# Optimization experiments

Measured on AMD Instinct MI355X. Metric: run time of the kernel, lower is better.

## Reference

```python
import jax, jax.numpy as jnp
import numpy as np

GRAPH_DIM = 512
LLM_DIM = 4096
N_HEADS = 8
D_KEYS = 128
DK_H = N_HEADS * D_KEYS  # 1024


def setup_inputs() -> dict:
    key = jax.random.key(0)
    ks = jax.random.split(key, 12)
    B, L, S = 8, 1024, 1000
    sc = 0.02
    return {
        "target_embedding": jax.random.normal(ks[0], (B, L, GRAPH_DIM), jnp.float32),
        "source_embedding": jax.random.normal(ks[1], (S, LLM_DIM), jnp.float32),
        "value_embedding": jax.random.normal(ks[2], (S, LLM_DIM), jnp.float32),
        # weights stored as [in, out] (pre-transposed vs torch Linear)
        "Wq": jax.random.normal(ks[3], (GRAPH_DIM, DK_H), jnp.float32) * sc,
        "bq": jnp.zeros((DK_H,), jnp.float32),
        "Wk": jax.random.normal(ks[4], (LLM_DIM, DK_H), jnp.float32) * sc,
        "bk": jnp.zeros((DK_H,), jnp.float32),
        "Wv": jax.random.normal(ks[5], (LLM_DIM, DK_H), jnp.float32) * sc,
        "bv": jnp.zeros((DK_H,), jnp.float32),
        "Wo": jax.random.normal(ks[6], (DK_H, LLM_DIM), jnp.float32) * sc,
        "bo": jnp.zeros((LLM_DIM,), jnp.float32),
    }


def reference(target_embedding, source_embedding, value_embedding,
              Wq, bq, Wk, bk, Wv, bv, Wo, bo):
    B, L, _ = target_embedding.shape
    S, _ = source_embedding.shape
    H, E = N_HEADS, D_KEYS
    q = (target_embedding @ Wq + bq).reshape(B, L, H, E)   # blhe
    k = (source_embedding @ Wk + bk).reshape(S, H, E)      # she (batch-shared)
    v = (value_embedding @ Wv + bv).reshape(S, H, E)       # she (batch-shared)
    scale = 1.0 / jnp.sqrt(jnp.asarray(E, q.dtype))
    scores = jnp.einsum('blhe,she->bhls', q, k)            # [B,H,L,S]
    A = jax.nn.softmax(scale * scores, axis=-1)            # dropout = identity (eval)
    out = jnp.einsum('bhls,she->blhe', A, v).reshape(B, L, H * E)
    return out @ Wo + bo                                   # [B,L,llm_dim]
```

## Files before the change

kernel.cpp:

```cpp
#include <hip/hip_runtime.h>
#include <cstdint>
#include <cstddef>

typedef __bf16 bf16;
typedef __bf16 bf16x4 __attribute__((ext_vector_type(4)));
typedef __bf16 bf16x8 __attribute__((ext_vector_type(8)));
typedef float f32x4 __attribute__((ext_vector_type(4)));


__device__ __forceinline__ void gload_lds16(const void* g, void* l) {
    typedef __attribute__((address_space(1))) void gv;
    typedef __attribute__((address_space(3))) void lv;
    __builtin_amdgcn_global_load_lds((gv*)g, (lv*)l, 16, 0, 0);
}

__global__ __launch_bounds__(256) void cast3_f32_bf16(
    const float* __restrict__ in0, bf16* __restrict__ out0,
    const float* __restrict__ in1, bf16* __restrict__ out1,
    const float* __restrict__ in2, bf16* __restrict__ out2)
{
    const int which = blockIdx.y;
    const float* in = which == 0 ? in0 : which == 1 ? in1 : in2;
    bf16* out       = which == 0 ? out0 : which == 1 ? out1 : out2;
    const size_t n_in = which == 0 ? (size_t)8192 * 512 : (size_t)1000 * 4096;

    const size_t i = ((size_t)blockIdx.x * 256 + threadIdx.x) * 8;
    f32x4 a = (f32x4){0.f, 0.f, 0.f, 0.f};
    f32x4 b = (f32x4){0.f, 0.f, 0.f, 0.f};
    if (i < n_in) {
        a = *(const f32x4*)(in + i);
        b = *(const f32x4*)(in + i + 4);
    }
    bf16x8 o;
    o[0] = (bf16)a[0]; o[1] = (bf16)a[1]; o[2] = (bf16)a[2]; o[3] = (bf16)a[3];
    o[4] = (bf16)b[0]; o[5] = (bf16)b[1]; o[6] = (bf16)b[2]; o[7] = (bf16)b[3];
    *(bf16x8*)(out + i) = o;
}

__global__ __launch_bounds__(256) void transpose_cast(
    const float* __restrict__ in, bf16* __restrict__ out, int R, int C)
{
    __shared__ bf16 tile[32][33];
    const int tx = threadIdx.x & 31, ty = threadIdx.x >> 5;
    const int c0 = blockIdx.x * 32, r0 = blockIdx.y * 32;
    #pragma unroll
    for (int i = ty; i < 32; i += 8)
        tile[i][tx] = (bf16)in[(size_t)(r0 + i) * C + (c0 + tx)];
    __syncthreads();
    #pragma unroll
    for (int i = ty; i < 32; i += 8)
        out[(size_t)(c0 + i) * R + (r0 + tx)] = tile[tx][i];
}

__global__ __launch_bounds__(256) void gemm_bt(
    const bf16* __restrict__ A, const bf16* __restrict__ Bt,
    const float* __restrict__ bias, void* __restrict__ Cv,
    int M, int N, int K, int lda, int ldb, int ldc, int outF32)
{
    __shared__ __align__(16) bf16 As[128 * 32];
    __shared__ __align__(16) bf16 Bs[128 * 32];

    const int tid = threadIdx.x;
    const int w = tid >> 6, ln = tid & 63;
    const int bm = blockIdx.y, bn = blockIdx.x;
    const int wm = (w >> 1) * 64, wn = (w & 1) * 64;
    const int rgrp = ln >> 4, cl = ln & 15;

    f32x4 acc[4][4];
    #pragma unroll
    for (int mt = 0; mt < 4; ++mt)
        #pragma unroll
        for (int nt = 0; nt < 4; ++nt)
            acc[mt][nt] = (f32x4){0.f, 0.f, 0.f, 0.f};

    for (int k0 = 0; k0 < K; k0 += 32) {
        #pragma unroll
        for (int j = 0; j < 2; ++j) {
            const int t2 = tid + 256 * j;
            int arow = bm * 128 + (t2 >> 2);
            if (arow > M - 1) arow = M - 1;
            const bf16* ag = A + (size_t)arow * lda + k0 + (t2 & 3) * 8;
            gload_lds16(ag, (char*)As + j * 4096 + w * 1024);
            const int brow = bn * 128 + (t2 >> 2);
            const bf16* bg = Bt + (size_t)brow * ldb + k0 + (t2 & 3) * 8;
            gload_lds16(bg, (char*)Bs + j * 4096 + w * 1024);
        }
        __syncthreads();

        bf16x8 af[4], bfr[4];
        #pragma unroll
        for (int mt = 0; mt < 4; ++mt)
            af[mt] = *(const bf16x8*)(As + (wm + mt * 16 + cl) * 32 + rgrp * 8);
        #pragma unroll
        for (int nt = 0; nt < 4; ++nt)
            bfr[nt] = *(const bf16x8*)(Bs + (wn + nt * 16 + cl) * 32 + rgrp * 8);
        #pragma unroll
        for (int mt = 0; mt < 4; ++mt)
            #pragma unroll
            for (int nt = 0; nt < 4; ++nt)
                acc[mt][nt] = __builtin_amdgcn_mfma_f32_16x16x32_bf16(
                    bfr[nt], af[mt], acc[mt][nt], 0, 0, 0);
        __syncthreads();
    }

    #pragma unroll
    for (int nt = 0; nt < 4; ++nt) {
        const int col0 = bn * 128 + wn + nt * 16 + rgrp * 4;
        const f32x4 bv4 = bias ? *(const f32x4*)(bias + col0)
                               : (f32x4){0.f, 0.f, 0.f, 0.f};
        #pragma unroll
        for (int mt = 0; mt < 4; ++mt) {
            const int row = bm * 128 + wm + mt * 16 + cl;
            if (row < M) {
                const f32x4 v = acc[mt][nt] + bv4;
                if (outF32) {
                    __builtin_nontemporal_store(
                        v, (f32x4*)((float*)Cv + (size_t)row * ldc + col0));
                } else {
                    bf16x4 h;
                    h[0] = (bf16)v[0]; h[1] = (bf16)v[1];
                    h[2] = (bf16)v[2]; h[3] = (bf16)v[3];
                    *(bf16x4*)((bf16*)Cv + (size_t)row * ldc + col0) = h;
                }
            }
        }
    }
}

__global__ __launch_bounds__(256) void gemm_kv(
    const bf16* __restrict__ A0, const bf16* __restrict__ Bt0,
    const float* __restrict__ b0, bf16* __restrict__ C0,
    const bf16* __restrict__ A1, const bf16* __restrict__ Bt1,
    const float* __restrict__ b1, bf16* __restrict__ C1)
{
    const int sel = blockIdx.z;
    const bf16* A  = sel ? A1 : A0;
    const bf16* Bt = sel ? Bt1 : Bt0;
    const float* bias = sel ? b1 : b0;
    bf16* Cv = sel ? C1 : C0;
    const int transC = sel;
    const int M = 1024, K = 4096, lda = 4096, ldb = 4096, ldc = 1024;

    __shared__ __align__(16) bf16 As[64 * 64];
    __shared__ __align__(16) bf16 Bs[64 * 64];

    const int tid = threadIdx.x;
    const int w = tid >> 6, ln = tid & 63;
    const int bm = blockIdx.y, bn = blockIdx.x;
    const int wm = (w >> 1) * 32, wn = (w & 1) * 32;
    const int rgrp = ln >> 4, cl = ln & 15;

    f32x4 acc[2][2];
    #pragma unroll
    for (int mt = 0; mt < 2; ++mt)
        #pragma unroll
        for (int nt = 0; nt < 2; ++nt)
            acc[mt][nt] = (f32x4){0.f, 0.f, 0.f, 0.f};

    for (int k0 = 0; k0 < K; k0 += 64) {
        #pragma unroll
        for (int j = 0; j < 2; ++j) {
            const int arow = bm * 64 + j * 32 + w * 8 + (ln >> 3);
            const bf16* ag = A + (size_t)arow * lda + k0 + (ln & 7) * 8;
            gload_lds16(ag, (char*)As + j * 4096 + w * 1024);
            const int brow = bn * 64 + j * 32 + w * 8 + (ln >> 3);
            const bf16* bg = Bt + (size_t)brow * ldb + k0 + (ln & 7) * 8;
            gload_lds16(bg, (char*)Bs + j * 4096 + w * 1024);
        }
        __syncthreads();

        bf16x8 af[2][2], bfr[2][2];
        #pragma unroll
        for (int mt = 0; mt < 2; ++mt)
            #pragma unroll
            for (int kk = 0; kk < 2; ++kk)
                af[mt][kk] = *(const bf16x8*)(As + (wm + mt * 16 + cl) * 64 + kk * 32 + rgrp * 8);
        #pragma unroll
        for (int nt = 0; nt < 2; ++nt)
            #pragma unroll
            for (int kk = 0; kk < 2; ++kk)
                bfr[nt][kk] = *(const bf16x8*)(Bs + (wn + nt * 16 + cl) * 64 + kk * 32 + rgrp * 8);
        #pragma unroll
        for (int mt = 0; mt < 2; ++mt)
            #pragma unroll
            for (int nt = 0; nt < 2; ++nt)
                #pragma unroll
                for (int kk = 0; kk < 2; ++kk)
                    acc[mt][nt] = __builtin_amdgcn_mfma_f32_16x16x32_bf16(
                        af[mt][kk], bfr[nt][kk], acc[mt][nt], 0, 0, 0);
        __syncthreads();
    }

    #pragma unroll
    for (int nt = 0; nt < 2; ++nt) {
        const int col = bn * 64 + wn + nt * 16 + cl;
        const float bvv = bias[col];
        #pragma unroll
        for (int mt = 0; mt < 2; ++mt) {
            #pragma unroll
            for (int reg = 0; reg < 4; ++reg) {
                const int row = bm * 64 + wm + mt * 16 + rgrp * 4 + reg;
                const float v = acc[mt][nt][reg] + bvv;
                const size_t idx = transC ? (size_t)col * ldc + row
                                          : (size_t)row * ldc + col;
                Cv[idx] = (bf16)v;
            }
        }
    }
}

__global__ __launch_bounds__(256) void flash_attn(
    const bf16* __restrict__ Q, const bf16* __restrict__ Kb,
    const bf16* __restrict__ Vt, bf16* __restrict__ O)
{
    const int tid = threadIdx.x;
    const int w = tid >> 6, ln = tid & 63;
    const int b = blockIdx.x >> 3, h = blockIdx.x & 7;
    const int l0 = blockIdx.y * 128 + w * 32;
    const int rgrp = ln >> 4, cl = ln & 15;
    const float sl2 = 0.08838834764831845f * 1.44269504088896340736f;

    __shared__ __align__(16) bf16 Ks[2][32 * 128];
    __shared__ __align__(16) bf16 Vs[2][128 * 32];
    __shared__ __align__(16) bf16 Pl[4][2][16 * 40];

    bf16x8 qf[2][4];
    #pragma unroll
    for (int m = 0; m < 2; ++m) {
        const bf16* qp = Q + (size_t)(b * 1024 + l0 + m * 16 + cl) * 1024 + h * 128 + rgrp * 8;
        #pragma unroll
        for (int kk = 0; kk < 4; ++kk) qf[m][kk] = *(const bf16x8*)(qp + kk * 32);
    }

    f32x4 o[2][8];
    #pragma unroll
    for (int m = 0; m < 2; ++m)
        #pragma unroll
        for (int nt = 0; nt < 8; ++nt) o[m][nt] = (f32x4){0.f, 0.f, 0.f, 0.f};
    float m_[2] = {-1e30f, -1e30f};
    float l_[2] = {0.f, 0.f};

    auto stage = [&](int bi, int t) {
        const int s0 = t * 32;
        #pragma unroll
        for (int c = 0; c < 2; ++c) {
            {
                const int r = c * 16 + w * 4 + (ln >> 4);
                const int e = ((ln & 15) ^ (r & 7)) << 3;
                gload_lds16(Kb + (size_t)(s0 + r) * 1024 + h * 128 + e,
                            (char*)Ks[bi] + c * 4096 + w * 1024);
            }
            {
                const int r = c * 64 + w * 16 + (ln >> 2);
                const int sc = ((ln & 3) ^ (r & 3)) << 3;
                gload_lds16(Vt + (size_t)(h * 128 + r) * 1024 + s0 + sc,
                            (char*)Vs[bi] + c * 4096 + w * 1024);
            }
        }
    };

    stage(0, 0);

    for (int t = 0; t < 32; ++t) {
        __syncthreads();
        if (t < 31) stage((t + 1) & 1, t + 1);
        const int bi = t & 1;
        const int s0 = t * 32;
        const bf16* Kt = Ks[bi];
        const bf16* Vtl = Vs[bi];

        bf16x8 kf[2][4];
        #pragma unroll
        for (int half = 0; half < 2; ++half) {
            const int row = half * 16 + cl;
            #pragma unroll
            for (int kk = 0; kk < 4; ++kk) {
                const int pos = (kk * 4 + rgrp) ^ (row & 7);
                kf[half][kk] = *(const bf16x8*)((const char*)Kt + row * 256 + pos * 16);
            }
        }

        f32x4 st[2][2];
        #pragma unroll
        for (int m = 0; m < 2; ++m)
            #pragma unroll
            for (int half = 0; half < 2; ++half) {
                f32x4 sc = (f32x4){0.f, 0.f, 0.f, 0.f};
                #pragma unroll
                for (int kk = 0; kk < 4; ++kk)
                    sc = __builtin_amdgcn_mfma_f32_16x16x32_bf16(
                        kf[half][kk], qf[m][kk], sc, 0, 0, 0);
                st[m][half] = sc;
            }

        #pragma unroll
        for (int m = 0; m < 2; ++m) {
            float z[8];
            #pragma unroll
            for (int half = 0; half < 2; ++half)
                #pragma unroll
                for (int reg = 0; reg < 4; ++reg) {
                    const int sg = s0 + half * 16 + rgrp * 4 + reg;
                    z[half * 4 + reg] = (sg < 1000) ? st[m][half][reg] * sl2 : -1e30f;
                }
            float mx = fmaxf(fmaxf(fmaxf(z[0], z[1]), fmaxf(z[2], z[3])),
                             fmaxf(fmaxf(z[4], z[5]), fmaxf(z[6], z[7])));
            mx = fmaxf(mx, __shfl_xor(mx, 16));
            mx = fmaxf(mx, __shfl_xor(mx, 32));
            if (__any(mx > m_[m] + 8.0f)) {
                const float mnew = fmaxf(m_[m], mx);
                const float alpha = __builtin_amdgcn_exp2f(m_[m] - mnew);
                m_[m] = mnew;
                l_[m] *= alpha;
                #pragma unroll
                for (int reg = 0; reg < 4; ++reg) {
                    const float ar = __shfl(alpha, rgrp * 4 + reg);
                    #pragma unroll
                    for (int nt = 0; nt < 8; ++nt) o[m][nt][reg] *= ar;
                }
            }
            float p[8];
            float rs = 0.f;
            #pragma unroll
            for (int i = 0; i < 8; ++i) {
                p[i] = __builtin_amdgcn_exp2f(z[i] - m_[m]);
                rs += p[i];
            }
            rs += __shfl_xor(rs, 16);
            rs += __shfl_xor(rs, 32);
            l_[m] += rs;
            #pragma unroll
            for (int half = 0; half < 2; ++half) {
                bf16x4 pk;
                #pragma unroll
                for (int reg = 0; reg < 4; ++reg) pk[reg] = (bf16)p[half * 4 + reg];
                *(bf16x4*)(&Pl[w][m][cl * 40 + half * 16 + rgrp * 4]) = pk;
            }
        }

        bf16x8 vf[8];
        #pragma unroll
        for (int nt = 0; nt < 8; ++nt) {
            const int row = nt * 16 + cl;
            const int pos = rgrp ^ (row & 3);
            vf[nt] = *(const bf16x8*)((const char*)Vtl + row * 64 + pos * 16);
        }

        #pragma unroll
        for (int m = 0; m < 2; ++m) {
            const bf16x8 pa = *(const bf16x8*)(&Pl[w][m][cl * 40 + rgrp * 8]);
            #pragma unroll
            for (int nt = 0; nt < 8; ++nt)
                o[m][nt] = __builtin_amdgcn_mfma_f32_16x16x32_bf16(
                    pa, vf[nt], o[m][nt], 0, 0, 0);
        }
    }

    #pragma unroll
    for (int m = 0; m < 2; ++m) {
        #pragma unroll
        for (int reg = 0; reg < 4; ++reg) {
            const float inv = __builtin_amdgcn_rcpf(__shfl(l_[m], rgrp * 4 + reg));
            const int row = l0 + m * 16 + rgrp * 4 + reg;
            #pragma unroll
            for (int nt = 0; nt < 8; ++nt) {
                const int col = h * 128 + nt * 16 + cl;
                O[(size_t)(b * 1024 + row) * 1024 + col] = (bf16)(o[m][nt][reg] * inv);
            }
        }
    }
}

extern "C" void kernel_launch(void* const* d_in, const int* in_sizes, int n_in,
                              void* d_out, int out_size, void* d_ws, size_t ws_size,
                              hipStream_t stream)
{
    const float* target = (const float*)d_in[0];
    const float* source = (const float*)d_in[1];
    const float* value  = (const float*)d_in[2];
    const float* Wq = (const float*)d_in[3];
    const float* bq = (const float*)d_in[4];
    const float* Wk = (const float*)d_in[5];
    const float* bk = (const float*)d_in[6];
    const float* Wv = (const float*)d_in[7];
    const float* bv = (const float*)d_in[8];
    const float* Wo = (const float*)d_in[9];
    const float* bo = (const float*)d_in[10];

    char* po = (char*)d_out;
    size_t off = 0;
    bf16* tgt_b = (bf16*)(po + off); off += (size_t)8192 * 512 * 2;
    bf16* src_b = (bf16*)(po + off); off += (size_t)1024 * 4096 * 2;
    bf16* val_b = (bf16*)(po + off); off += (size_t)1024 * 4096 * 2;
    bf16* WqT   = (bf16*)(po + off); off += (size_t)1024 * 512 * 2;
    bf16* WkT   = (bf16*)(po + off); off += (size_t)1024 * 4096 * 2;
    bf16* WvT   = (bf16*)(po + off); off += (size_t)1024 * 4096 * 2;
    bf16* Qb    = (bf16*)(po + off); off += (size_t)8192 * 1024 * 2;
    bf16* Kb    = (bf16*)(po + off); off += (size_t)1024 * 1024 * 2;
    bf16* Vt    = (bf16*)(po + off); off += (size_t)1024 * 1024 * 2;
    char* ws = (char*)d_ws;
    bf16* AO  = (bf16*)ws;
    bf16* WoT = (bf16*)(ws + (size_t)8192 * 1024 * 2);

    cast3_f32_bf16<<<dim3(2048, 3), 256, 0, stream>>>(
        target, tgt_b, source, src_b, value, val_b);

    transpose_cast<<<dim3(32, 16), 256, 0, stream>>>(Wq, WqT, 512, 1024);
    transpose_cast<<<dim3(32, 128), 256, 0, stream>>>(Wk, WkT, 4096, 1024);
    transpose_cast<<<dim3(32, 128), 256, 0, stream>>>(Wv, WvT, 4096, 1024);
    transpose_cast<<<dim3(128, 32), 256, 0, stream>>>(Wo, WoT, 1024, 4096);

    gemm_bt<<<dim3(8, 64), 256, 0, stream>>>(tgt_b, WqT, bq, Qb, 8192, 1024, 512, 512, 512, 1024, 0);
    gemm_kv<<<dim3(16, 16, 2), 256, 0, stream>>>(
        src_b, WkT, bk, Kb, val_b, WvT, bv, Vt);

    flash_attn<<<dim3(64, 8), 256, 0, stream>>>(Qb, Kb, Vt, AO);

    gemm_bt<<<dim3(32, 64), 256, 0, stream>>>(AO, WoT, bo, d_out, 8192, 4096, 1024, 1024, 1024, 4096, 1);

    (void)in_sizes; (void)n_in; (void)out_size; (void)ws_size;
}
```

Baseline: 444.0 us.

## Deepen GEMM K-tile with swizzled LDS, XCD block remap, fuse transposes, setprio

The projection GEMM now loads a 64-wide K slice per iteration into XOR-swizzled LDS, halving barrier count and avoiding bank conflicts. It also remaps block indices so neighbouring tiles land on the same XCD for L2 reuse. The four weight transpose launches are merged into one kernel to cut launch overhead. Launch bounds hints are added, and s_setprio raises wave priority around the MFMA sections in flash attention. Doubling LDS per block may reduce occupancy.

```diff
diff --git a/kernel.cpp b/kernel.cpp
--- a/kernel.cpp
+++ b/kernel.cpp
@@ -37,12 +37,22 @@
     *(bf16x8*)(out + i) = o;
 }
 
-__global__ __launch_bounds__(256) void transpose_cast(
-    const float* __restrict__ in, bf16* __restrict__ out, int R, int C)
-{
+__global__ __launch_bounds__(256) void transpose4(
+    const float* __restrict__ Wq, bf16* __restrict__ WqT,
+    const float* __restrict__ Wk, bf16* __restrict__ WkT,
+    const float* __restrict__ Wv, bf16* __restrict__ WvT,
+    const float* __restrict__ Wo, bf16* __restrict__ WoT)
+{
+    int id = blockIdx.x;
+    const float* in; bf16* out; int R, C, bx, by;
+    if (id < 512)       { in = Wq; out = WqT; R = 512;  C = 1024; bx = id % 32;  by = id / 32; }
+    else if (id < 4608) { id -= 512;  in = Wk; out = WkT; R = 4096; C = 1024; bx = id % 32;  by = id / 32; }
+    else if (id < 8704) { id -= 4608; in = Wv; out = WvT; R = 4096; C = 1024; bx = id % 32;  by = id / 32; }
+    else                { id -= 8704; in = Wo; out = WoT; R = 1024; C = 4096; bx = id % 128; by = id / 128; }
+
     __shared__ bf16 tile[32][33];
     const int tx = threadIdx.x & 31, ty = threadIdx.x >> 5;
-    const int c0 = blockIdx.x * 32, r0 = blockIdx.y * 32;
+    const int c0 = bx * 32, r0 = by * 32;
     #pragma unroll
     for (int i = ty; i < 32; i += 8)
         tile[i][tx] = (bf16)in[(size_t)(r0 + i) * C + (c0 + tx)];
@@ -52,17 +62,31 @@
         out[(size_t)(c0 + i) * R + (r0 + tx)] = tile[tx][i];
 }
 
-__global__ __launch_bounds__(256) void gemm_bt(
+__global__ __launch_bounds__(256, 3) void gemm_bt(
     const bf16* __restrict__ A, const bf16* __restrict__ Bt,
     const float* __restrict__ bias, void* __restrict__ Cv,
     int M, int N, int K, int lda, int ldb, int ldc, int outF32)
 {
-    __shared__ __align__(16) bf16 As[128 * 32];
-    __shared__ __align__(16) bf16 Bs[128 * 32];
+    __shared__ __align__(16) bf16 As[128 * 64];
+    __shared__ __align__(16) bf16 Bs[128 * 64];
 
     const int tid = threadIdx.x;
     const int w = tid >> 6, ln = tid & 63;
-    const int bm = blockIdx.y, bn = blockIdx.x;
+
+    const int gx = gridDim.x, gy = gridDim.y;
+    int bm, bn;
+    if (((gx & 7) | (gy & 7)) == 0) {
+        const int orig = blockIdx.y * gx + blockIdx.x;
+        const int xcd = orig & 7, t = orig >> 3;
+        const int nsb_x = gx >> 3;
+        const int s = xcd + 8 * (t >> 6);
+        const int win = t & 63;
+        bm = (s / nsb_x) * 8 + (win >> 3);
+        bn = (s % nsb_x) * 8 + (win & 7);
+    } else {
+        bm = blockIdx.y; bn = blockIdx.x;
+    }
+
     const int wm = (w >> 1) * 64, wn = (w & 1) * 64;
     const int rgrp = ln >> 4, cl = ln & 15;
 
@@ -73,33 +97,44 @@
         for (int nt = 0; nt < 4; ++nt)
             acc[mt][nt] = (f32x4){0.f, 0.f, 0.f, 0.f};
 
-    for (int k0 = 0; k0 < K; k0 += 32) {
-        #pragma unroll
-        for (int j = 0; j < 2; ++j) {
+    for (int k0 = 0; k0 < K; k0 += 64) {
+        #pragma unroll
+        for (int j = 0; j < 4; ++j) {
             const int t2 = tid + 256 * j;
-            int arow = bm * 128 + (t2 >> 2);
+            const int row = t2 >> 3;
+            const int ch = (t2 & 7) ^ (row & 7);
+            int arow = bm * 128 + row;
             if (arow > M - 1) arow = M - 1;
-            const bf16* ag = A + (size_t)arow * lda + k0 + (t2 & 3) * 8;
-            gload_lds16(ag, (char*)As + j * 4096 + w * 1024);
-            const int brow = bn * 128 + (t2 >> 2);
-            const bf16* bg = Bt + (size_t)brow * ldb + k0 + (t2 & 3) * 8;
-            gload_lds16(bg, (char*)Bs + j * 4096 + w * 1024);
+            gload_lds16(A + (size_t)arow * lda + k0 + ch * 8,
+                        (char*)As + j * 4096 + w * 1024);
+            const int brow = bn * 128 + row;
+            gload_lds16(Bt + (size_t)brow * ldb + k0 + ch * 8,
+                        (char*)Bs + j * 4096 + w * 1024);
         }
         __syncthreads();
 
-        bf16x8 af[4], bfr[4];
-        #pragma unroll
-        for (int mt = 0; mt < 4; ++mt)
-            af[mt] = *(const bf16x8*)(As + (wm + mt * 16 + cl) * 32 + rgrp * 8);
-        #pragma unroll
-        for (int nt = 0; nt < 4; ++nt)
-            bfr[nt] = *(const bf16x8*)(Bs + (wn + nt * 16 + cl) * 32 + rgrp * 8);
-        #pragma unroll
-        for (int mt = 0; mt < 4; ++mt)
-            #pragma unroll
-            for (int nt = 0; nt < 4; ++nt)
-                acc[mt][nt] = __builtin_amdgcn_mfma_f32_16x16x32_bf16(
-                    bfr[nt], af[mt], acc[mt][nt], 0, 0, 0);
+        #pragma unroll
+        for (int kk = 0; kk < 2; ++kk) {
+            bf16x8 af[4], bfr[4];
+            #pragma unroll
+            for (int mt = 0; mt < 4; ++mt) {
+                const int row = wm + mt * 16 + cl;
+                const int ch = (kk * 4 + rgrp) ^ (row & 7);
+                af[mt] = *(const bf16x8*)(As + row * 64 + ch * 8);
+            }
+            #pragma unroll
+            for (int nt = 0; nt < 4; ++nt) {
+                const int row = wn + nt * 16 + cl;
+                const int ch = (kk * 4 + rgrp) ^ (row & 7);
+                bfr[nt] = *(const bf16x8*)(Bs + row * 64 + ch * 8);
+            }
+            #pragma unroll
+            for (int mt = 0; mt < 4; ++mt)
+                #pragma unroll
+                for (int nt = 0; nt < 4; ++nt)
+                    acc[mt][nt] = __builtin_amdgcn_mfma_f32_16x16x32_bf16(
+                        bfr[nt], af[mt], acc[mt][nt], 0, 0, 0);
+        }
         __syncthreads();
     }
 
@@ -127,7 +162,7 @@
     }
 }
 
-__global__ __launch_bounds__(256) void gemm_kv(
+__global__ __launch_bounds__(256, 4) void gemm_kv(
     const bf16* __restrict__ A0, const bf16* __restrict__ Bt0,
     const float* __restrict__ b0, bf16* __restrict__ C0,
     const bf16* __restrict__ A1, const bf16* __restrict__ Bt1,
@@ -139,7 +174,7 @@
     const float* bias = sel ? b1 : b0;
     bf16* Cv = sel ? C1 : C0;
     const int transC = sel;
-    const int M = 1024, K = 4096, lda = 4096, ldb = 4096, ldc = 1024;
+    const int K = 4096, lda = 4096, ldb = 4096, ldc = 1024;
 
     __shared__ __align__(16) bf16 As[64 * 64];
     __shared__ __align__(16) bf16 Bs[64 * 64];
@@ -281,6 +316,7 @@
         }
 
         f32x4 st[2][2];
+        __builtin_amdgcn_s_setprio(1);
         #pragma unroll
         for (int m = 0; m < 2; ++m)
             #pragma unroll
@@ -292,6 +328,7 @@
                         kf[half][kk], qf[m][kk], sc, 0, 0, 0);
                 st[m][half] = sc;
             }
+        __builtin_amdgcn_s_setprio(0);
 
         #pragma unroll
         for (int m = 0; m < 2; ++m) {
@@ -346,6 +383,7 @@
             vf[nt] = *(const bf16x8*)((const char*)Vtl + row * 64 + pos * 16);
         }
 
+        __builtin_amdgcn_s_setprio(1);
         #pragma unroll
         for (int m = 0; m < 2; ++m) {
             const bf16x8 pa = *(const bf16x8*)(&Pl[w][m][cl * 40 + rgrp * 8]);
@@ -354,6 +392,7 @@
                 o[m][nt] = __builtin_amdgcn_mfma_f32_16x16x32_bf16(
                     pa, vf[nt], o[m][nt], 0, 0, 0);
         }
+        __builtin_amdgcn_s_setprio(0);
     }
 
     #pragma unroll
@@ -405,10 +444,7 @@
     cast3_f32_bf16<<<dim3(2048, 3), 256, 0, stream>>>(
         target, tgt_b, source, src_b, value, val_b);
 
-    transpose_cast<<<dim3(32, 16), 256, 0, stream>>>(Wq, WqT, 512, 1024);
-    transpose_cast<<<dim3(32, 128), 256, 0, stream>>>(Wk, WkT, 4096, 1024);
-    transpose_cast<<<dim3(32, 128), 256, 0, stream>>>(Wv, WvT, 4096, 1024);
-    transpose_cast<<<dim3(128, 32), 256, 0, stream>>>(Wo, WoT, 1024, 4096);
+    transpose4<<<12800, 256, 0, stream>>>(Wq, WqT, Wk, WkT, Wv, WvT, Wo, WoT);
 
     gemm_bt<<<dim3(8, 64), 256, 0, stream>>>(tgt_b, WqT, bq, Qb, 8192, 1024, 512, 512, 512, 1024, 0);
     gemm_kv<<<dim3(16, 16, 2), 256, 0, stream>>>(
```

New measurement: 454.3 us. 2.3% more time.
